# Kernel optimization log

Hardware: AMD Instinct MI355X
Metric: run time of the kernel (lower is better)

## Reference

```python
import jax, jax.numpy as jnp
import numpy as np

B, S, E, D, M = 512, 64, 768, 256, 3  # batch, seq, encoder_dim, dim, num_modalities


def setup_inputs() -> dict:
    key = jax.random.key(0)
    ks = jax.random.split(key, 16)
    inp = {}
    for i in range(M):
        inp[f"latent{i}"] = jax.random.normal(ks[i], (B, S, E), dtype=jnp.float32)
        inp[f"Wp{i}"] = jax.random.normal(ks[3 + i], (D, E), dtype=jnp.float32) * (1.0 / np.sqrt(E))
        inp[f"bp{i}"] = jnp.zeros((D,), dtype=jnp.float32)
    inp["corr"] = jax.random.uniform(ks[7], (D, D), dtype=jnp.float32, minval=-0.1, maxval=0.1)
    F_in = 2 * D * (M - 1)  # 1024
    inp["Wb"] = jax.random.normal(ks[8], (64, F_in), dtype=jnp.float32) * (1.0 / np.sqrt(F_in))
    inp["bb"] = jnp.zeros((64,), dtype=jnp.float32)
    inp["gamma"] = jnp.ones((64,), dtype=jnp.float32)
    inp["beta"] = jnp.zeros((64,), dtype=jnp.float32)
    return inp


def _forward(latents, Wps, bps, corr, Wb, bb, gamma, beta):
    # project each modality: [B,S,E] -> [B,S,D]
    proj = [lat @ Wp.T + bp for lat, Wp, bp in zip(latents, Wps, bps)]
    anchor = proj[0]
    pairs = []
    for other in proj[1:]:
        # cc[b,i,j] = anchor[b,i,:] @ corr @ other[b,j,:]
        cc = jnp.einsum('bid,de,bje->bij', anchor, corr, other)
        a_att = jax.nn.softmax(cc, axis=1)   # softmax over anchor tokens
        o_att = jax.nn.softmax(cc, axis=2)   # softmax over other tokens (= softmax(cc^T, dim=1))
        att_anchor = jnp.einsum('bid,bij->bdj', anchor, a_att) + jnp.swapaxes(anchor, 1, 2)
        att_other = jnp.einsum('bjd,bij->bdi', other, o_att) + jnp.swapaxes(other, 1, 2)
        pairs.append(jnp.concatenate([att_anchor, att_other], axis=1))  # [B,2D,S]
    fused = jnp.concatenate(pairs, axis=1)          # [B, 2D(M-1), S]
    fused = jnp.swapaxes(fused, 1, 2)               # [B, S, 2D(M-1)]
    h = fused @ Wb.T + bb                           # [B, S, 64]
    mu = jnp.mean(h, axis=-1, keepdims=True)
    var = jnp.var(h, axis=-1, keepdims=True)
    h = (h - mu) / jnp.sqrt(var + 1e-5) * gamma + beta
    return jax.nn.relu(h)


def reference(latent0, latent1, latent2, Wp0, bp0, Wp1, bp1, Wp2, bp2, corr, Wb, bb, gamma, beta):
    return _forward([latent0, latent1, latent2], [Wp0, Wp1, Wp2], [bp0, bp1, bp2],
                    corr, Wb, bb, gamma, beta)
```

## Files before the change

### kernel.cpp

```cpp
#include <hip/hip_runtime.h>
#include <hip/hip_bf16.h>
#include <stdint.h>

#define Bsz 512
#define Ssz 64
#define Esz 768
#define Dsz 256
#define MROWS (Bsz * Ssz)
#define FIN 1024

typedef _Float16 f16;
typedef f16 f16x4 __attribute__((ext_vector_type(4)));
typedef f16 f16x8v __attribute__((ext_vector_type(8)));
typedef float f32x4 __attribute__((ext_vector_type(4)));
typedef short bf16x8 __attribute__((ext_vector_type(8)));

__device__ __forceinline__ uint32_t f2bf(float f) {
    uint32_t u = __float_as_uint(f);
    u += 0x7fffu + ((u >> 16) & 1u);
    return u >> 16;
}

__global__ __launch_bounds__(256) void prep(const float* __restrict__ Wp0,
                                            const float* __restrict__ Wp1,
                                            const float* __restrict__ Wp2,
                                            const float* __restrict__ corr,
                                            const float* __restrict__ Wb,
                                            f16* __restrict__ Wph,
                                            f16* __restrict__ corrT,
                                            uint16_t* __restrict__ Wbh) {
    const int t = blockIdx.x * 256 + threadIdx.x;
    if (t < 3 * 196608) {
        const int z = t / 196608, i = t % 196608;
        const float* W = (z == 0) ? Wp0 : (z == 1) ? Wp1 : Wp2;
        Wph[(size_t)z * 196608 + i] = (f16)W[i];
    }
    if (t < 65536) {
        const int d = t >> 8, e = t & 255;
        corrT[e * 256 + d] = (f16)corr[d * 256 + e];
        Wbh[t] = (uint16_t)f2bf(Wb[t]);
    }
}

template <bool A_F16, bool BIAS>
__global__ __launch_bounds__(256) void mfma_gemm(
    const float* __restrict__ A32a, const float* __restrict__ A32b,
    const float* __restrict__ A32c, const f16* __restrict__ A16,
    const f16* __restrict__ Bh, const float* __restrict__ biasA,
    const float* __restrict__ biasB, const float* __restrict__ biasC,
    f16* __restrict__ Ch, int K) {
    const int tid = threadIdx.x;
    const int n0 = blockIdx.x * 128;
    const int m0 = blockIdx.y * 128;
    const int z = blockIdx.z;
    const float* A32 = (z == 0) ? A32a : (z == 1) ? A32b : A32c;
    const float* bias = (z == 0) ? biasA : (z == 1) ? biasB : biasC;
    const f16* Bz = Bh + (size_t)z * 256 * K;
    f16* Cz = Ch + (size_t)z * MROWS * 256;

    __shared__ __align__(16) f16 AhS[8192];
    __shared__ __align__(16) f16 BhS[8192];

    const int lane = tid & 63;
    const int w = tid >> 6;
    const int ma = (w >> 1) * 4;
    const int nb = (w & 1) * 4;

    const int srow = tid >> 3;
    const int sc8 = tid & 7;

    f32x4 acc[4][4];
#pragma unroll
    for (int i = 0; i < 4; i++)
#pragma unroll
        for (int j = 0; j < 4; j++) acc[i][j] = (f32x4){0.f, 0.f, 0.f, 0.f};

    for (int k0 = 0; k0 < K; k0 += 64) {
        __syncthreads();
#pragma unroll
        for (int r = 0; r < 4; r++) {
            const int row = srow + 32 * r;
            const int unit = (((sc8 >> 2) * 8 + (row >> 4)) * 64 + (row & 15) + 16 * (sc8 & 3)) ^ (sc8 & 3);
            if constexpr (A_F16) {
                uint4 av = *(const uint4*)(A16 + (size_t)(m0 + row) * K + k0 + sc8 * 8);
                *(uint4*)&AhS[unit * 8] = av;
            } else {
                const float* p = A32 + (size_t)(m0 + row) * K + k0 + sc8 * 8;
                float4 lo = *(const float4*)p;
                float4 hi = *(const float4*)(p + 4);
                f16x8v h;
                h[0] = (f16)lo.x; h[1] = (f16)lo.y; h[2] = (f16)lo.z; h[3] = (f16)lo.w;
                h[4] = (f16)hi.x; h[5] = (f16)hi.y; h[6] = (f16)hi.z; h[7] = (f16)hi.w;
                *(f16x8v*)&AhS[unit * 8] = h;
            }
            uint4 bv = *(const uint4*)(Bz + (size_t)(n0 + row) * K + k0 + sc8 * 8);
            *(uint4*)&BhS[unit * 8] = bv;
        }
        __syncthreads();
#pragma unroll
        for (int kh = 0; kh < 2; kh++) {
            f16x8v af[4], bf[4];
#pragma unroll
            for (int i = 0; i < 4; i++)
                af[i] = *(const f16x8v*)&AhS[((((kh * 8 + ma + i) * 64 + lane)) ^ (lane >> 4)) * 8];
#pragma unroll
            for (int j = 0; j < 4; j++)
                bf[j] = *(const f16x8v*)&BhS[((((kh * 8 + nb + j) * 64 + lane)) ^ (lane >> 4)) * 8];
#pragma unroll
            for (int i = 0; i < 4; i++)
#pragma unroll
                for (int j = 0; j < 4; j++)
                    acc[i][j] = __builtin_amdgcn_mfma_f32_16x16x32_f16(af[i], bf[j], acc[i][j], 0, 0, 0);
        }
    }

    f16* Ce = AhS;
    __syncthreads();
    const int cr = lane & 15, qr = lane >> 4;
    const int mwl = (w >> 1) * 64;
    const int nwl = (w & 1) * 64;
#pragma unroll
    for (int i = 0; i < 4; i++) {
#pragma unroll
        for (int j = 0; j < 4; j++) {
            const int col = nwl + j * 16 + cr;
            const float bv = BIAS ? bias[n0 + col] : 0.f;
#pragma unroll
            for (int r = 0; r < 4; r++) {
                const int row = mwl + i * 16 + qr * 4 + r;
                Ce[row * 128 + col] = (f16)(acc[i][j][r] + bv);
            }
        }
    }
    __syncthreads();
#pragma unroll
    for (int r = 0; r < 8; r++) {
        const int f = r * 256 + tid;
        const int row = f >> 4, c16 = f & 15;
        uint4 v = *(const uint4*)&Ce[row * 128 + c16 * 8];
        *(uint4*)(Cz + (size_t)(m0 + row) * 256 + n0 + c16 * 8) = v;
    }
}

__global__ __launch_bounds__(256) void cc_softmax(const f16* __restrict__ ac,
                                                  const f16* __restrict__ proj1,
                                                  const f16* __restrict__ proj2,
                                                  float* __restrict__ a_att,
                                                  float* __restrict__ o_att) {
    const int b = blockIdx.x, q = blockIdx.y;
    const f16* __restrict__ A = ac + (size_t)b * Ssz * Dsz;
    const f16* __restrict__ Bp = (q ? proj2 : proj1) + (size_t)b * Ssz * Dsz;
    __shared__ float sc[64][65];
    __shared__ float cmax[64], csum[64], rmax[64], rsum[64];
    const int tid = threadIdx.x;
    const int lane = tid & 63, w = tid >> 6;
    const int lr = lane & 15;
    const int lk = lane >> 4;

    f32x4 acc[4];
#pragma unroll
    for (int j = 0; j < 4; j++) acc[j] = (f32x4){0.f, 0.f, 0.f, 0.f};

    const f16* __restrict__ Arow = A + (size_t)(w * 16 + lr) * Dsz + lk * 8;
    for (int ks = 0; ks < 8; ks++) {
        f16x8v af = *(const f16x8v*)(Arow + ks * 32);
        f16x8v bf[4];
#pragma unroll
        for (int j = 0; j < 4; j++)
            bf[j] = *(const f16x8v*)(Bp + (size_t)(j * 16 + lr) * Dsz + ks * 32 + lk * 8);
#pragma unroll
        for (int j = 0; j < 4; j++)
            acc[j] = __builtin_amdgcn_mfma_f32_16x16x32_f16(af, bf[j], acc[j], 0, 0, 0);
    }
#pragma unroll
    for (int j = 0; j < 4; j++)
#pragma unroll
        for (int r = 0; r < 4; r++) sc[w * 16 + lk * 4 + r][j * 16 + lr] = acc[j][r];
    __syncthreads();
    if (tid < 64) {
        const int j = tid;
        float m = -1e30f;
        for (int i = 0; i < 64; i++) m = fmaxf(m, sc[i][j]);
        float s = 0.f;
        for (int i = 0; i < 64; i++) s += __expf(sc[i][j] - m);
        cmax[j] = m;
        csum[j] = s;
    } else if (tid < 128) {
        const int i = tid - 64;
        float m = -1e30f;
        for (int j = 0; j < 64; j++) m = fmaxf(m, sc[i][j]);
        float s = 0.f;
        for (int j = 0; j < 64; j++) s += __expf(sc[i][j] - m);
        rmax[i] = m;
        rsum[i] = s;
    }
    __syncthreads();
    const int j = tid & 63;
    const int i00 = tid >> 6;
    float* __restrict__ ap = a_att + (size_t)(q * Bsz + b) * Ssz * Ssz;
    float* __restrict__ op = o_att + (size_t)(q * Bsz + b) * Ssz * Ssz;
    const float cm = cmax[j];
    const float ci = 1.f / csum[j];
    for (int i = i00; i < 64; i += 4) {
        const float v = sc[i][j];
        ap[i * 64 + j] = __expf(v - cm) * ci;
        op[i * 64 + j] = __expf(v - rmax[i]) / rsum[i];
    }
}

__global__ __launch_bounds__(256) void attn_apply(const f16* __restrict__ proj0,
                                                  const f16* __restrict__ proj1,
                                                  const f16* __restrict__ proj2,
                                                  const float* __restrict__ a_att,
                                                  const float* __restrict__ o_att,
                                                  uint16_t* __restrict__ fused) {
    const int b = blockIdx.x, q = blockIdx.y;
    const f16* __restrict__ anchor = proj0 + (size_t)b * Ssz * Dsz;
    const f16* __restrict__ other = (q ? proj2 : proj1) + (size_t)b * Ssz * Dsz;
    __shared__ __align__(16) float att[64][68];
    __shared__ __align__(16) float Bs[16][256];
    const int tid = threadIdx.x;
    const int tx = tid & 31;
    const int ty = tid >> 5;

    for (int part = 0; part < 2; part++) {
        const float4* __restrict__ attg =
            (const float4*)((part == 0 ? a_att : o_att) + (size_t)(q * Bsz + b) * 4096);
        const f16* __restrict__ Bmat = (part == 0) ? anchor : other;
        __syncthreads();
#pragma unroll
        for (int t = tid, r = 0; r < 4; t += 256, r++) {
            float4 v = attg[t];
            const int i = t >> 4, j4 = (t & 15) * 4;
            if (part == 0) {
                att[i][j4 + 0] = v.x;
                att[i][j4 + 1] = v.y;
                att[i][j4 + 2] = v.z;
                att[i][j4 + 3] = v.w;
            } else {
                att[j4 + 0][i] = v.x;
                att[j4 + 1][i] = v.y;
                att[j4 + 2][i] = v.z;
                att[j4 + 3][i] = v.w;
            }
        }
        float acc[8][8];
#pragma unroll
        for (int i = 0; i < 8; i++)
#pragma unroll
            for (int j = 0; j < 8; j++) acc[i][j] = 0.f;

        for (int k0 = 0; k0 < 64; k0 += 16) {
            f16x4 bvr[4];
#pragma unroll
            for (int t = tid, r = 0; r < 4; t += 256, r++)
                bvr[r] = *(const f16x4*)(Bmat + (size_t)((t >> 6) + k0) * Dsz + (t & 63) * 4);
            __syncthreads();
#pragma unroll
            for (int t = tid, r = 0; r < 4; t += 256, r++) {
                float4 fv;
                fv.x = (float)bvr[r].x;
                fv.y = (float)bvr[r].y;
                fv.z = (float)bvr[r].z;
                fv.w = (float)bvr[r].w;
                *(float4*)&Bs[t >> 6][(t & 63) * 4] = fv;
            }
            __syncthreads();
#pragma unroll
            for (int k = 0; k < 16; k++) {
                const int kk = k0 + k;
                float4 a0 = *(const float4*)&att[kk][ty * 8];
                float4 a1 = *(const float4*)&att[kk][ty * 8 + 4];
                float4 b0 = *(const float4*)&Bs[k][tx * 8];
                float4 b1 = *(const float4*)&Bs[k][tx * 8 + 4];
                float a_[8] = {a0.x, a0.y, a0.z, a0.w, a1.x, a1.y, a1.z, a1.w};
                float b_[8] = {b0.x, b0.y, b0.z, b0.w, b1.x, b1.y, b1.z, b1.w};
#pragma unroll
                for (int i = 0; i < 8; i++)
#pragma unroll
                    for (int j = 0; j < 8; j++) acc[i][j] = fmaf(a_[i], b_[j], acc[i][j]);
            }
        }
        const int c0 = q * 512 + part * 256 + tx * 8;
#pragma unroll
        for (int r = 0; r < 8; r++) {
            const int s = ty * 8 + r;
            f16x8v rv = *(const f16x8v*)(Bmat + (size_t)s * Dsz + tx * 8);
            uint4 pk;
            pk.x = f2bf(acc[r][0] + (float)rv[0]) | (f2bf(acc[r][1] + (float)rv[1]) << 16);
            pk.y = f2bf(acc[r][2] + (float)rv[2]) | (f2bf(acc[r][3] + (float)rv[3]) << 16);
            pk.z = f2bf(acc[r][4] + (float)rv[4]) | (f2bf(acc[r][5] + (float)rv[5]) << 16);
            pk.w = f2bf(acc[r][6] + (float)rv[6]) | (f2bf(acc[r][7] + (float)rv[7]) << 16);
            *(uint4*)(fused + (size_t)(b * 64 + s) * FIN + c0) = pk;
        }
    }
}

__global__ __launch_bounds__(256) void final_gemm_ln(const uint16_t* __restrict__ fused,
                                                     const uint16_t* __restrict__ Wbh,
                                                     const float* __restrict__ bb,
                                                     const float* __restrict__ gamma,
                                                     const float* __restrict__ beta,
                                                     float* __restrict__ out) {
    const int m0 = blockIdx.x * 128;
    const int tid = threadIdx.x;
    const int lane = tid & 63, w = tid >> 6;
    const int lr = lane & 15;
    const int lk = lane >> 4;

    f32x4 acc[2][4];
#pragma unroll
    for (int mi = 0; mi < 2; mi++)
#pragma unroll
        for (int jf = 0; jf < 4; jf++) acc[mi][jf] = (f32x4){0.f, 0.f, 0.f, 0.f};

    const uint16_t* __restrict__ A0 = fused + (size_t)(m0 + w * 32 + lr) * FIN + lk * 8;
    const uint16_t* __restrict__ B0 = Wbh + (size_t)lr * FIN + lk * 8;

    for (int ks = 0; ks < 32; ks++) {
        bf16x8 af[2], bf[4];
#pragma unroll
        for (int mi = 0; mi < 2; mi++)
            af[mi] = *(const bf16x8*)(A0 + (size_t)mi * 16 * FIN + ks * 32);
#pragma unroll
        for (int jf = 0; jf < 4; jf++)
            bf[jf] = *(const bf16x8*)(B0 + (size_t)jf * 16 * FIN + ks * 32);
#pragma unroll
        for (int mi = 0; mi < 2; mi++)
#pragma unroll
            for (int jf = 0; jf < 4; jf++)
                acc[mi][jf] = __builtin_amdgcn_mfma_f32_16x16x32_bf16(af[mi], bf[jf], acc[mi][jf], 0, 0, 0);
    }

    float bbv[4], gv[4], bv2[4];
#pragma unroll
    for (int jf = 0; jf < 4; jf++) {
        const int c = jf * 16 + lr;
        bbv[jf] = bb[c];
        gv[jf] = gamma[c];
        bv2[jf] = beta[c];
    }
#pragma unroll
    for (int mi = 0; mi < 2; mi++) {
#pragma unroll
        for (int r = 0; r < 4; r++) {
            float h[4];
            float s1 = 0.f, s2 = 0.f;
#pragma unroll
            for (int jf = 0; jf < 4; jf++) {
                h[jf] = acc[mi][jf][r] + bbv[jf];
                s1 += h[jf];
                s2 += h[jf] * h[jf];
            }
#pragma unroll
            for (int m = 1; m < 16; m <<= 1) {
                s1 += __shfl_xor(s1, m);
                s2 += __shfl_xor(s2, m);
            }
            const float mu = s1 * (1.f / 64.f);
            const float inv = rsqrtf(s2 * (1.f / 64.f) - mu * mu + 1e-5f);
            const int row = m0 + w * 32 + mi * 16 + lk * 4 + r;
#pragma unroll
            for (int jf = 0; jf < 4; jf++) {
                const float v = (h[jf] - mu) * inv * gv[jf] + bv2[jf];
                out[(size_t)row * 64 + jf * 16 + lr] = fmaxf(v, 0.f);
            }
        }
    }
}

extern "C" void kernel_launch(void* const* d_in, const int* in_sizes, int n_in,
                              void* d_out, int out_size, void* d_ws, size_t ws_size,
                              hipStream_t stream) {
    const float* latent0 = (const float*)d_in[0];
    const float* Wp0 = (const float*)d_in[1];
    const float* bp0 = (const float*)d_in[2];
    const float* latent1 = (const float*)d_in[3];
    const float* Wp1 = (const float*)d_in[4];
    const float* bp1 = (const float*)d_in[5];
    const float* latent2 = (const float*)d_in[6];
    const float* Wp2 = (const float*)d_in[7];
    const float* bp2 = (const float*)d_in[8];
    const float* corr = (const float*)d_in[9];
    const float* Wb = (const float*)d_in[10];
    const float* bb = (const float*)d_in[11];
    const float* gamma = (const float*)d_in[12];
    const float* beta = (const float*)d_in[13];

    char* ws = (char*)d_ws;
    f16* proj_h = (f16*)ws;
    f16* ac_h = (f16*)(ws + 48ull * 1024 * 1024);
    float* a_att = (float*)(ws + 64ull * 1024 * 1024);
    float* o_att = (float*)(ws + 80ull * 1024 * 1024);
    uint16_t* fused = (uint16_t*)(ws + 96ull * 1024 * 1024);
    f16* Wph = (f16*)(ws + 160ull * 1024 * 1024);
    f16* corrT = (f16*)(ws + 162ull * 1024 * 1024);
    uint16_t* Wbh = (uint16_t*)(ws + 162ull * 1024 * 1024 + 128ull * 1024);

    float* out = (float*)d_out;
    dim3 blk(256);

    prep<<<2304, blk, 0, stream>>>(Wp0, Wp1, Wp2, corr, Wb, Wph, corrT, Wbh);

    mfma_gemm<false, true><<<dim3(2, 256, 3), blk, 0, stream>>>(
        latent0, latent1, latent2, (const f16*)nullptr, Wph, bp0, bp1, bp2, proj_h, Esz);

    mfma_gemm<true, false><<<dim3(2, 256, 1), blk, 0, stream>>>(
        (const float*)nullptr, (const float*)nullptr, (const float*)nullptr, proj_h,
        corrT, (const float*)nullptr, (const float*)nullptr, (const float*)nullptr,
        ac_h, Dsz);

    const f16* proj1_h = proj_h + (size_t)MROWS * 256;
    const f16* proj2_h = proj_h + 2ull * MROWS * 256;

    cc_softmax<<<dim3(Bsz, 2), blk, 0, stream>>>(ac_h, proj1_h, proj2_h, a_att, o_att);

    attn_apply<<<dim3(Bsz, 2), blk, 0, stream>>>(proj_h, proj1_h, proj2_h, a_att, o_att, fused);

    final_gemm_ln<<<MROWS / 128, blk, 0, stream>>>(fused, Wbh, bb, gamma, beta, out);

    (void)in_sizes; (void)n_in; (void)out_size; (void)ws_size;
}
```

Before: 479.6 us.

## Reassociate attention-apply with bottleneck projection and prefetch GEMM tiles into registers

The final linear layer is moved ahead of the attention apply: each modality projection is first multiplied by its slice of Wb (G = Wb_slice · X), then the attention matrices are applied to these small 64x64 results and the residual is added from G. This replaces the large fused [B,S,1024] intermediate and the scalar-FMA attention kernel with two small MFMA kernels. Attention weights are also stored as f16 rather than fp32, and the projection GEMM now prefetches the next K tile into registers while computing the current one. The cost is lower precision, since Wb and the attention weights become f16, and more register pressure in the GEMM.

```diff
diff --git a/kernel.cpp b/kernel.cpp
--- a/kernel.cpp
+++ b/kernel.cpp
@@ -13,13 +13,6 @@
 typedef f16 f16x4 __attribute__((ext_vector_type(4)));
 typedef f16 f16x8v __attribute__((ext_vector_type(8)));
 typedef float f32x4 __attribute__((ext_vector_type(4)));
-typedef short bf16x8 __attribute__((ext_vector_type(8)));
-
-__device__ __forceinline__ uint32_t f2bf(float f) {
-    uint32_t u = __float_as_uint(f);
-    u += 0x7fffu + ((u >> 16) & 1u);
-    return u >> 16;
-}
 
 __global__ __launch_bounds__(256) void prep(const float* __restrict__ Wp0,
                                             const float* __restrict__ Wp1,
@@ -28,7 +21,7 @@
                                             const float* __restrict__ Wb,
                                             f16* __restrict__ Wph,
                                             f16* __restrict__ corrT,
-                                            uint16_t* __restrict__ Wbh) {
+                                            f16* __restrict__ Wbh) {
     const int t = blockIdx.x * 256 + threadIdx.x;
     if (t < 3 * 196608) {
         const int z = t / 196608, i = t % 196608;
@@ -38,7 +31,7 @@
     if (t < 65536) {
         const int d = t >> 8, e = t & 255;
         corrT[e * 256 + d] = (f16)corr[d * 256 + e];
-        Wbh[t] = (uint16_t)f2bf(Wb[t]);
+        Wbh[t] = (f16)Wb[t];
     }
 }
 
@@ -75,6 +68,27 @@
 #pragma unroll
         for (int j = 0; j < 4; j++) acc[i][j] = (f32x4){0.f, 0.f, 0.f, 0.f};
 
+    float4 alo[4], ahi[4];
+    uint4 a16r[4];
+    uint4 br[4];
+
+    auto loadk = [&](int kk) {
+#pragma unroll
+        for (int r = 0; r < 4; r++) {
+            const int row = srow + 32 * r;
+            if constexpr (A_F16) {
+                a16r[r] = *(const uint4*)(A16 + (size_t)(m0 + row) * K + kk + sc8 * 8);
+            } else {
+                const float* p = A32 + (size_t)(m0 + row) * K + kk + sc8 * 8;
+                alo[r] = *(const float4*)p;
+                ahi[r] = *(const float4*)(p + 4);
+            }
+            br[r] = *(const uint4*)(Bz + (size_t)(n0 + row) * K + kk + sc8 * 8);
+        }
+    };
+
+    loadk(0);
+
     for (int k0 = 0; k0 < K; k0 += 64) {
         __syncthreads();
 #pragma unroll
@@ -82,21 +96,19 @@
             const int row = srow + 32 * r;
             const int unit = (((sc8 >> 2) * 8 + (row >> 4)) * 64 + (row & 15) + 16 * (sc8 & 3)) ^ (sc8 & 3);
             if constexpr (A_F16) {
-                uint4 av = *(const uint4*)(A16 + (size_t)(m0 + row) * K + k0 + sc8 * 8);
-                *(uint4*)&AhS[unit * 8] = av;
+                *(uint4*)&AhS[unit * 8] = a16r[r];
             } else {
-                const float* p = A32 + (size_t)(m0 + row) * K + k0 + sc8 * 8;
-                float4 lo = *(const float4*)p;
-                float4 hi = *(const float4*)(p + 4);
                 f16x8v h;
-                h[0] = (f16)lo.x; h[1] = (f16)lo.y; h[2] = (f16)lo.z; h[3] = (f16)lo.w;
-                h[4] = (f16)hi.x; h[5] = (f16)hi.y; h[6] = (f16)hi.z; h[7] = (f16)hi.w;
+                h[0] = (f16)alo[r].x; h[1] = (f16)alo[r].y; h[2] = (f16)alo[r].z; h[3] = (f16)alo[r].w;
+                h[4] = (f16)ahi[r].x; h[5] = (f16)ahi[r].y; h[6] = (f16)ahi[r].z; h[7] = (f16)ahi[r].w;
                 *(f16x8v*)&AhS[unit * 8] = h;
             }
-            uint4 bv = *(const uint4*)(Bz + (size_t)(n0 + row) * K + k0 + sc8 * 8);
-            *(uint4*)&BhS[unit * 8] = bv;
+            *(uint4*)&BhS[unit * 8] = br[r];
         }
         __syncthreads();
+        const int kn = (k0 + 64 < K) ? (k0 + 64) : k0;
+        loadk(kn);
+        __builtin_amdgcn_sched_barrier(0);
 #pragma unroll
         for (int kh = 0; kh < 2; kh++) {
             f16x8v af[4], bf[4];
@@ -145,8 +157,8 @@
 __global__ __launch_bounds__(256) void cc_softmax(const f16* __restrict__ ac,
                                                   const f16* __restrict__ proj1,
                                                   const f16* __restrict__ proj2,
-                                                  float* __restrict__ a_att,
-                                                  float* __restrict__ o_att) {
+                                                  f16* __restrict__ aT,
+                                                  f16* __restrict__ oP) {
     const int b = blockIdx.x, q = blockIdx.y;
     const f16* __restrict__ A = ac + (size_t)b * Ssz * Dsz;
     const f16* __restrict__ Bp = (q ? proj2 : proj1) + (size_t)b * Ssz * Dsz;
@@ -195,176 +207,150 @@
         rsum[i] = s;
     }
     __syncthreads();
-    const int j = tid & 63;
-    const int i00 = tid >> 6;
-    float* __restrict__ ap = a_att + (size_t)(q * Bsz + b) * Ssz * Ssz;
-    float* __restrict__ op = o_att + (size_t)(q * Bsz + b) * Ssz * Ssz;
-    const float cm = cmax[j];
-    const float ci = 1.f / csum[j];
-    for (int i = i00; i < 64; i += 4) {
-        const float v = sc[i][j];
-        ap[i * 64 + j] = __expf(v - cm) * ci;
-        op[i * 64 + j] = __expf(v - rmax[i]) / rsum[i];
-    }
-}
-
-__global__ __launch_bounds__(256) void attn_apply(const f16* __restrict__ proj0,
-                                                  const f16* __restrict__ proj1,
-                                                  const f16* __restrict__ proj2,
-                                                  const float* __restrict__ a_att,
-                                                  const float* __restrict__ o_att,
-                                                  uint16_t* __restrict__ fused) {
-    const int b = blockIdx.x, q = blockIdx.y;
-    const f16* __restrict__ anchor = proj0 + (size_t)b * Ssz * Dsz;
-    const f16* __restrict__ other = (q ? proj2 : proj1) + (size_t)b * Ssz * Dsz;
-    __shared__ __align__(16) float att[64][68];
-    __shared__ __align__(16) float Bs[16][256];
-    const int tid = threadIdx.x;
-    const int tx = tid & 31;
-    const int ty = tid >> 5;
-
-    for (int part = 0; part < 2; part++) {
-        const float4* __restrict__ attg =
-            (const float4*)((part == 0 ? a_att : o_att) + (size_t)(q * Bsz + b) * 4096);
-        const f16* __restrict__ Bmat = (part == 0) ? anchor : other;
-        __syncthreads();
-#pragma unroll
-        for (int t = tid, r = 0; r < 4; t += 256, r++) {
-            float4 v = attg[t];
-            const int i = t >> 4, j4 = (t & 15) * 4;
-            if (part == 0) {
-                att[i][j4 + 0] = v.x;
-                att[i][j4 + 1] = v.y;
-                att[i][j4 + 2] = v.z;
-                att[i][j4 + 3] = v.w;
-            } else {
-                att[j4 + 0][i] = v.x;
-                att[j4 + 1][i] = v.y;
-                att[j4 + 2][i] = v.z;
-                att[j4 + 3][i] = v.w;
+    const int lid = tid & 63;
+    const int grp = tid >> 6;
+    f16* __restrict__ apT = aT + (size_t)(q * Bsz + b) * 4096;
+    f16* __restrict__ opR = oP + (size_t)(q * Bsz + b) * 4096;
+    for (int i = grp; i < 64; i += 4) {
+        const float v = __expf(sc[i][lid] - rmax[i]) / rsum[i];
+        opR[i * 64 + lid] = (f16)v;
+    }
+    for (int jj = grp; jj < 64; jj += 4) {
+        const float v = __expf(sc[lid][jj] - cmax[jj]) / csum[jj];
+        apT[jj * 64 + lid] = (f16)v;
+    }
+}
+
+__global__ __launch_bounds__(256) void g_gemm(const f16* __restrict__ proj,
+                                              const f16* __restrict__ Wbh,
+                                              f16* __restrict__ G) {
+    const int b = blockIdx.x;
+    const int tid = threadIdx.x, lane = tid & 63, w = tid >> 6;
+    const int q = w >> 1, part = w & 1;
+    const int z = part ? (1 + q) : 0;
+    const f16* __restrict__ X = proj + ((size_t)z * MROWS + b * 64) * 256;
+    const f16* __restrict__ Wc = Wbh + q * 512 + part * 256;
+    const int lr = lane & 15, lk = lane >> 4;
+
+    f32x4 acc[4][4];
+#pragma unroll
+    for (int i = 0; i < 4; i++)
+#pragma unroll
+        for (int j = 0; j < 4; j++) acc[i][j] = (f32x4){0.f, 0.f, 0.f, 0.f};
+
+    for (int ks = 0; ks < 8; ks++) {
+        f16x8v af[4], bf[4];
+#pragma unroll
+        for (int mi = 0; mi < 4; mi++)
+            af[mi] = *(const f16x8v*)(Wc + (size_t)(mi * 16 + lr) * FIN + ks * 32 + lk * 8);
+#pragma unroll
+        for (int nj = 0; nj < 4; nj++)
+            bf[nj] = *(const f16x8v*)(X + (size_t)(nj * 16 + lr) * 256 + ks * 32 + lk * 8);
+#pragma unroll
+        for (int mi = 0; mi < 4; mi++)
+#pragma unroll
+            for (int nj = 0; nj < 4; nj++)
+                acc[mi][nj] = __builtin_amdgcn_mfma_f32_16x16x32_f16(af[mi], bf[nj], acc[mi][nj], 0, 0, 0);
+    }
+
+    __shared__ __align__(16) f16 Gs[4][4096];
+#pragma unroll
+    for (int mi = 0; mi < 4; mi++)
+#pragma unroll
+        for (int nj = 0; nj < 4; nj++)
+#pragma unroll
+            for (int r = 0; r < 4; r++)
+                Gs[w][(mi * 16 + lk * 4 + r) * 64 + nj * 16 + lr] = (f16)acc[mi][nj][r];
+    __syncthreads();
+#pragma unroll
+    for (int r = 0; r < 8; r++) {
+        const int u = r * 64 + lane;
+        *(uint4*)(G + ((size_t)(b * 4 + w)) * 4096 + u * 8) = *(const uint4*)&Gs[w][u * 8];
+    }
+}
+
+__global__ __launch_bounds__(256) void attn_ln(const f16* __restrict__ aT,
+                                               const f16* __restrict__ oP,
+                                               const f16* __restrict__ G,
+                                               const float* __restrict__ bb,
+                                               const float* __restrict__ gamma,
+                                               const float* __restrict__ beta,
+                                               float* __restrict__ out) {
+    const int b = blockIdx.x;
+    const int tid = threadIdx.x, lane = tid & 63, w = tid >> 6;
+    const int lr = lane & 15, lk = lane >> 4;
+
+    __shared__ __align__(16) f16 Gs[4][4096];
+#pragma unroll
+    for (int r = 0; r < 8; r++) {
+        const int gu = r * 256 + tid;
+        const int term = gu >> 9, u = gu & 511;
+        const int o = u >> 3, tch = u & 7;
+        uint4 v = *(const uint4*)(G + ((size_t)(b * 4 + term)) * 4096 + u * 8);
+        const int su = o * 8 + (tch ^ (o & 7));
+        *(uint4*)&Gs[term][su * 8] = v;
+    }
+    __syncthreads();
+
+    f32x4 acc[4];
+#pragma unroll
+    for (int j = 0; j < 4; j++) acc[j] = (f32x4){0.f, 0.f, 0.f, 0.f};
+
+#pragma unroll
+    for (int term = 0; term < 4; term++) {
+        const int q = term >> 1;
+        const f16* __restrict__ Abase =
+            ((term & 1) ? oP : aT) + ((size_t)(q * Bsz + b)) * 4096;
+#pragma unroll
+        for (int kh = 0; kh < 2; kh++) {
+            f16x8v af = *(const f16x8v*)(Abase + (size_t)(w * 16 + lr) * 64 + kh * 32 + lk * 8);
+#pragma unroll
+            for (int jf = 0; jf < 4; jf++) {
+                const int o = jf * 16 + lr;
+                const int su = o * 8 + ((kh * 4 + lk) ^ (o & 7));
+                f16x8v bf = *(const f16x8v*)&Gs[term][su * 8];
+                acc[jf] = __builtin_amdgcn_mfma_f32_16x16x32_f16(af, bf, acc[jf], 0, 0, 0);
             }
         }
-        float acc[8][8];
-#pragma unroll
-        for (int i = 0; i < 8; i++)
-#pragma unroll
-            for (int j = 0; j < 8; j++) acc[i][j] = 0.f;
-
-        for (int k0 = 0; k0 < 64; k0 += 16) {
-            f16x4 bvr[4];
-#pragma unroll
-            for (int t = tid, r = 0; r < 4; t += 256, r++)
-                bvr[r] = *(const f16x4*)(Bmat + (size_t)((t >> 6) + k0) * Dsz + (t & 63) * 4);
-            __syncthreads();
-#pragma unroll
-            for (int t = tid, r = 0; r < 4; t += 256, r++) {
-                float4 fv;
-                fv.x = (float)bvr[r].x;
-                fv.y = (float)bvr[r].y;
-                fv.z = (float)bvr[r].z;
-                fv.w = (float)bvr[r].w;
-                *(float4*)&Bs[t >> 6][(t & 63) * 4] = fv;
+    }
+
+    float bbv[4], gv[4], bv2[4];
+#pragma unroll
+    for (int jf = 0; jf < 4; jf++) {
+        const int o = jf * 16 + lr;
+        bbv[jf] = bb[o];
+        gv[jf] = gamma[o];
+        bv2[jf] = beta[o];
+    }
+#pragma unroll
+    for (int r = 0; r < 4; r++) {
+        const int s = w * 16 + lk * 4 + r;
+        float h[4];
+        float s1 = 0.f, s2 = 0.f;
+#pragma unroll
+        for (int jf = 0; jf < 4; jf++) {
+            const int o = jf * 16 + lr;
+            float resid = 0.f;
+#pragma unroll
+            for (int term = 0; term < 4; term++) {
+                const int su = o * 8 + ((s >> 3) ^ (o & 7));
+                resid += (float)Gs[term][su * 8 + (s & 7)];
             }
-            __syncthreads();
-#pragma unroll
-            for (int k = 0; k < 16; k++) {
-                const int kk = k0 + k;
-                float4 a0 = *(const float4*)&att[kk][ty * 8];
-                float4 a1 = *(const float4*)&att[kk][ty * 8 + 4];
-                float4 b0 = *(const float4*)&Bs[k][tx * 8];
-                float4 b1 = *(const float4*)&Bs[k][tx * 8 + 4];
-                float a_[8] = {a0.x, a0.y, a0.z, a0.w, a1.x, a1.y, a1.z, a1.w};
-                float b_[8] = {b0.x, b0.y, b0.z, b0.w, b1.x, b1.y, b1.z, b1.w};
-#pragma unroll
-                for (int i = 0; i < 8; i++)
-#pragma unroll
-                    for (int j = 0; j < 8; j++) acc[i][j] = fmaf(a_[i], b_[j], acc[i][j]);
-            }
-        }
-        const int c0 = q * 512 + part * 256 + tx * 8;
-#pragma unroll
-        for (int r = 0; r < 8; r++) {
-            const int s = ty * 8 + r;
-            f16x8v rv = *(const f16x8v*)(Bmat + (size_t)s * Dsz + tx * 8);
-            uint4 pk;
-            pk.x = f2bf(acc[r][0] + (float)rv[0]) | (f2bf(acc[r][1] + (float)rv[1]) << 16);
-            pk.y = f2bf(acc[r][2] + (float)rv[2]) | (f2bf(acc[r][3] + (float)rv[3]) << 16);
-            pk.z = f2bf(acc[r][4] + (float)rv[4]) | (f2bf(acc[r][5] + (float)rv[5]) << 16);
-            pk.w = f2bf(acc[r][6] + (float)rv[6]) | (f2bf(acc[r][7] + (float)rv[7]) << 16);
-            *(uint4*)(fused + (size_t)(b * 64 + s) * FIN + c0) = pk;
-        }
-    }
-}
-
-__global__ __launch_bounds__(256) void final_gemm_ln(const uint16_t* __restrict__ fused,
-                                                     const uint16_t* __restrict__ Wbh,
-                                                     const float* __restrict__ bb,
-                                                     const float* __restrict__ gamma,
-                                                     const float* __restrict__ beta,
-                                                     float* __restrict__ out) {
-    const int m0 = blockIdx.x * 128;
-    const int tid = threadIdx.x;
-    const int lane = tid & 63, w = tid >> 6;
-    const int lr = lane & 15;
-    const int lk = lane >> 4;
-
-    f32x4 acc[2][4];
-#pragma unroll
-    for (int mi = 0; mi < 2; mi++)
-#pragma unroll
-        for (int jf = 0; jf < 4; jf++) acc[mi][jf] = (f32x4){0.f, 0.f, 0.f, 0.f};
-
-    const uint16_t* __restrict__ A0 = fused + (size_t)(m0 + w * 32 + lr) * FIN + lk * 8;
-    const uint16_t* __restrict__ B0 = Wbh + (size_t)lr * FIN + lk * 8;
-
-    for (int ks = 0; ks < 32; ks++) {
-        bf16x8 af[2], bf[4];
-#pragma unroll
-        for (int mi = 0; mi < 2; mi++)
-            af[mi] = *(const bf16x8*)(A0 + (size_t)mi * 16 * FIN + ks * 32);
-#pragma unroll
-        for (int jf = 0; jf < 4; jf++)
-            bf[jf] = *(const bf16x8*)(B0 + (size_t)jf * 16 * FIN + ks * 32);
-#pragma unroll
-        for (int mi = 0; mi < 2; mi++)
-#pragma unroll
-            for (int jf = 0; jf < 4; jf++)
-                acc[mi][jf] = __builtin_amdgcn_mfma_f32_16x16x32_bf16(af[mi], bf[jf], acc[mi][jf], 0, 0, 0);
-    }
-
-    float bbv[4], gv[4], bv2[4];
-#pragma unroll
-    for (int jf = 0; jf < 4; jf++) {
-        const int c = jf * 16 + lr;
-        bbv[jf] = bb[c];
-        gv[jf] = gamma[c];
-        bv2[jf] = beta[c];
-    }
-#pragma unroll
-    for (int mi = 0; mi < 2; mi++) {
-#pragma unroll
-        for (int r = 0; r < 4; r++) {
-            float h[4];
-            float s1 = 0.f, s2 = 0.f;
-#pragma unroll
-            for (int jf = 0; jf < 4; jf++) {
-                h[jf] = acc[mi][jf][r] + bbv[jf];
-                s1 += h[jf];
-                s2 += h[jf] * h[jf];
-            }
-#pragma unroll
-            for (int m = 1; m < 16; m <<= 1) {
-                s1 += __shfl_xor(s1, m);
-                s2 += __shfl_xor(s2, m);
-            }
-            const float mu = s1 * (1.f / 64.f);
-            const float inv = rsqrtf(s2 * (1.f / 64.f) - mu * mu + 1e-5f);
-            const int row = m0 + w * 32 + mi * 16 + lk * 4 + r;
-#pragma unroll
-            for (int jf = 0; jf < 4; jf++) {
-                const float v = (h[jf] - mu) * inv * gv[jf] + bv2[jf];
-                out[(size_t)row * 64 + jf * 16 + lr] = fmaxf(v, 0.f);
-            }
+            h[jf] = acc[jf][r] + resid + bbv[jf];
+            s1 += h[jf];
+            s2 += h[jf] * h[jf];
+        }
+#pragma unroll
+        for (int m = 1; m < 16; m <<= 1) {
+            s1 += __shfl_xor(s1, m);
+            s2 += __shfl_xor(s2, m);
+        }
+        const float mu = s1 * (1.f / 64.f);
+        const float inv = rsqrtf(s2 * (1.f / 64.f) - mu * mu + 1e-5f);
+#pragma unroll
+        for (int jf = 0; jf < 4; jf++) {
+            const float v = (h[jf] - mu) * inv * gv[jf] + bv2[jf];
+            out[(size_t)(b * 64 + s) * 64 + jf * 16 + lr] = fmaxf(v, 0.f);
         }
     }
 }
@@ -390,12 +376,12 @@
     char* ws = (char*)d_ws;
     f16* proj_h = (f16*)ws;
     f16* ac_h = (f16*)(ws + 48ull * 1024 * 1024);
-    float* a_att = (float*)(ws + 64ull * 1024 * 1024);
-    float* o_att = (float*)(ws + 80ull * 1024 * 1024);
-    uint16_t* fused = (uint16_t*)(ws + 96ull * 1024 * 1024);
+    f16* aT = (f16*)(ws + 64ull * 1024 * 1024);
+    f16* oP = (f16*)(ws + 72ull * 1024 * 1024);
+    f16* G = (f16*)(ws + 80ull * 1024 * 1024);
     f16* Wph = (f16*)(ws + 160ull * 1024 * 1024);
     f16* corrT = (f16*)(ws + 162ull * 1024 * 1024);
-    uint16_t* Wbh = (uint16_t*)(ws + 162ull * 1024 * 1024 + 128ull * 1024);
+    f16* Wbh = (f16*)(ws + 162ull * 1024 * 1024 + 128ull * 1024);
 
     float* out = (float*)d_out;
     dim3 blk(256);
@@ -413,11 +399,11 @@
     const f16* proj1_h = proj_h + (size_t)MROWS * 256;
     const f16* proj2_h = proj_h + 2ull * MROWS * 256;
 
-    cc_softmax<<<dim3(Bsz, 2), blk, 0, stream>>>(ac_h, proj1_h, proj2_h, a_att, o_att);
-
-    attn_apply<<<dim3(Bsz, 2), blk, 0, stream>>>(proj_h, proj1_h, proj2_h, a_att, o_att, fused);
-
-    final_gemm_ln<<<MROWS / 128, blk, 0, stream>>>(fused, Wbh, bb, gamma, beta, out);
+    cc_softmax<<<dim3(Bsz, 2), blk, 0, stream>>>(ac_h, proj1_h, proj2_h, aT, oP);
+
+    g_gemm<<<Bsz, blk, 0, stream>>>(proj_h, Wbh, G);
+
+    attn_ln<<<Bsz, blk, 0, stream>>>(aT, oP, G, bb, gamma, beta, out);
 
     (void)in_sizes; (void)n_in; (void)out_size; (void)ws_size;
 }
```

Measured after the change: 502.0 us. 1.05x slower.
